# Optimization experiments

Measured on AMD Instinct MI355X. Metric: run time of the kernel, lower is better.

Reference implementation:

```python
import jax, jax.numpy as jnp
import numpy as np

V, E, H = 50257, 256, 128          # vocab, embedding_size, lstm hidden per direction
L, B = 2048, 64                    # seq_len, batch (x is [L, B], seq-first)
SEP, MASK = 50256, 0
SEP_EVERY = 16
N_UTT = L // SEP_EVERY             # utterances per sequence (seps planted regularly)


def setup_inputs() -> dict:
    key = jax.random.key(0)
    ks = jax.random.split(key, 12)
    x = jax.random.randint(ks[0], (L, B), 0, SEP, dtype=jnp.int32)
    # plant sep tokens every SEP_EVERY positions -> each utterance has SEP_EVERY tokens
    x = x.at[SEP_EVERY - 1::SEP_EVERY, :].set(SEP)
    s = 1.0 / np.sqrt(H)
    u = lambda k, sh: jax.random.uniform(k, sh, jnp.float32, -s, s)
    return {
        "x": x,
        "emb": jax.random.normal(ks[1], (V, E), jnp.float32),
        "w_ih_f": u(ks[2], (4 * H, E)), "w_hh_f": u(ks[3], (4 * H, H)),
        "b_ih_f": u(ks[4], (4 * H,)),   "b_hh_f": u(ks[5], (4 * H,)),
        "w_ih_b": u(ks[6], (4 * H, E)), "w_hh_b": u(ks[7], (4 * H, H)),
        "b_ih_b": u(ks[8], (4 * H,)),   "b_hh_b": u(ks[9], (4 * H,)),
        "w_out": u(ks[10], (2, E)),     "b_out": u(ks[11], (2,)),
    }


def _lstm_dir(xu, w_ih, w_hh, b_ih, b_hh, reverse):
    # xu: [T, B, E]; PyTorch LSTM gate order i, f, g, o
    xp = jnp.einsum("tbe,ge->tbg", xu, w_ih) + b_ih + b_hh  # [T, B, 4H]

    def step(carry, xt):
        h, c = carry
        g = xt + h @ w_hh.T
        i, f, gg, o = jnp.split(g, 4, axis=-1)
        c = jax.nn.sigmoid(f) * c + jax.nn.sigmoid(i) * jnp.tanh(gg)
        h = jax.nn.sigmoid(o) * jnp.tanh(c)
        return (h, c), h

    init = (jnp.zeros((xu.shape[1], H), xu.dtype), jnp.zeros((xu.shape[1], H), xu.dtype))
    _, hs = jax.lax.scan(step, init, xp, reverse=reverse)
    return hs  # [T, B, H]


def _forward(x, emb, w_ih_f, w_hh_f, b_ih_f, b_hh_f, w_ih_b, w_hh_b, b_ih_b, b_hh_b, w_out, b_out):
    # --- ragged utterance mean-pool (replaces per-token Python loops) ---
    seps = (x == SEP)
    seg = jnp.cumsum(seps.astype(jnp.int32), axis=0) - seps.astype(jnp.int32)  # [L,B]: utterance id per token (sep ends its utterance)
    gids = (seg * B + jnp.arange(B, dtype=jnp.int32)[None, :]).reshape(L * B)
    tok_emb = emb[x]                                              # [L, B, E]
    sums = jax.ops.segment_sum(tok_emb.reshape(L * B, E), gids, num_segments=N_UTT * B).reshape(N_UTT, B, E)
    cnts = jax.ops.segment_sum(jnp.ones((L * B,), tok_emb.dtype), gids, num_segments=N_UTT * B).reshape(N_UTT, B, 1)
    u = jnp.where(cnts > 0, sums / jnp.maximum(cnts, 1.0), 0.0)   # [N_UTT, B, E] (zeros pad, as original)
    # --- BiLSTM over utterances ---
    h_f = _lstm_dir(u, w_ih_f, w_hh_f, b_ih_f, b_hh_f, reverse=False)
    h_b = _lstm_dir(u, w_ih_b, w_hh_b, b_ih_b, b_hh_b, reverse=True)
    h = jnp.concatenate([h_f, h_b], axis=-1)                      # [N_UTT, B, E]
    logits = jnp.einsum("tbe,oe->tbo", h, w_out) + b_out          # [N_UTT, B, 2]
    policy = jax.nn.softmax(logits, axis=-1)
    # greedy policy (deterministic reference)
    u_mask = jnp.argmax(policy, axis=-1)                          # [N_UTT, B] in {0,1}
    chosen_policy = jnp.take_along_axis(policy, u_mask[..., None], axis=-1)  # [N_UTT, B, 1]
    # expand utterance mask to token mask and mask the input
    token_mask = u_mask.astype(bool)[seg, jnp.arange(B)[None, :]]  # [L, B]
    masked_input = jnp.where(token_mask, x, MASK)
    return logits, policy, chosen_policy, u_mask.astype(bool), masked_input


def reference(x, emb, w_ih_f, w_hh_f, b_ih_f, b_hh_f, w_ih_b, w_hh_b, b_ih_b, b_hh_b, w_out, b_out):
    return _forward(x, emb, w_ih_f, w_hh_f, b_ih_f, b_hh_f, w_ih_b, w_hh_b, b_ih_b, b_hh_b, w_out, b_out)
```

## Files before the change

### kernel.cpp

```cpp
#include <hip/hip_runtime.h>
#include <hip/hip_fp16.h>
#include <math.h>

#define LL   2048
#define BB   64
#define EE   256
#define HH   128
#define GG   512
#define TT   128
#define SEPT 50256

__global__ __launch_bounds__(256) void segscan_k(
    const int* __restrict__ x, int* __restrict__ seg,
    int* __restrict__ cnt, int* __restrict__ start)
{
    int b   = blockIdx.x;
    int tid = threadIdx.x;
    __shared__ int tsum[256];
    __shared__ int ucnt[TT];
    __shared__ int ustart[TT];

    int flags[8];
    int local = 0;
#pragma unroll
    for (int i = 0; i < 8; i++) {
        int t = tid * 8 + i;
        flags[i] = (x[t * BB + b] == SEPT) ? 1 : 0;
        local += flags[i];
    }
    tsum[tid] = local;
    __syncthreads();
    int val = local;
    for (int off = 1; off < 256; off <<= 1) {
        int other = (tid >= off) ? tsum[tid - off] : 0;
        __syncthreads();
        val += other;
        tsum[tid] = val;
        __syncthreads();
    }
    int excl = val - local;

    if (tid < TT) ucnt[tid] = 0;
    __syncthreads();
    int run = excl;
#pragma unroll
    for (int i = 0; i < 8; i++) {
        int t = tid * 8 + i;
        int s = run;
        seg[t * BB + b] = s;
        run += flags[i];
        if (s < TT) atomicAdd(&ucnt[s], 1);
    }
    __syncthreads();
    if (tid == 0) {
        int acc = 0;
        for (int u = 0; u < TT; u++) { ustart[u] = acc; acc += ucnt[u]; }
    }
    __syncthreads();
    if (tid < TT) {
        cnt[tid * BB + b]   = ucnt[tid];
        start[tid * BB + b] = ustart[tid];
    }
}

__global__ __launch_bounds__(256) void pool_k(
    const int* __restrict__ x, const float* __restrict__ emb,
    const int* __restrict__ cnt, const int* __restrict__ start,
    float* __restrict__ up)
{
    int wid  = threadIdx.x >> 6;
    int lane = threadIdx.x & 63;
    int bid  = blockIdx.x * 4 + wid;
    int b    = bid & 63;
    int c    = cnt[bid];
    int st   = start[bid];

    float4 acc = {0.f, 0.f, 0.f, 0.f};
    int tok = (c > 0) ? x[st * BB + b] : 0;
    for (int j = 0; j < c; j++) {
        int tok_n = (j + 1 < c) ? x[(st + j + 1) * BB + b] : 0;
        float4 v = ((const float4*)(emb + (size_t)tok * EE))[lane];
        acc.x += v.x; acc.y += v.y; acc.z += v.z; acc.w += v.w;
        tok = tok_n;
    }
    float inv = (c > 0) ? 1.f / (float)c : 0.f;
    float4 r = {acc.x * inv, acc.y * inv, acc.z * inv, acc.w * inv};
    ((float4*)(up + (size_t)bid * EE))[lane] = r;
}

__global__ __launch_bounds__(256) void xp_gemm_k(
    const float* __restrict__ A,
    const float* __restrict__ wf, const float* __restrict__ wb,
    const float* __restrict__ bihf, const float* __restrict__ bhhf,
    const float* __restrict__ bihb, const float* __restrict__ bhhb,
    float* __restrict__ C)
{
    __shared__ float As[32][128];
    __shared__ float Bs[32][128];
    int tid  = threadIdx.x;
    int row0 = blockIdx.x * 128;
    int col0 = blockIdx.y * 128;
    int tx = tid & 15, ty = tid >> 4;
    float acc[8][8] = {};

    for (int k0 = 0; k0 < EE; k0 += 32) {
#pragma unroll
        for (int i = 0; i < 4; i++) {
            int idx = tid + i * 256;
            int m   = idx >> 3;
            int k4  = idx & 7;
            float4 av = *(const float4*)(A + (size_t)(row0 + m) * EE + k0 + k4 * 4);
            As[k4 * 4 + 0][m] = av.x; As[k4 * 4 + 1][m] = av.y;
            As[k4 * 4 + 2][m] = av.z; As[k4 * 4 + 3][m] = av.w;
        }
#pragma unroll
        for (int i = 0; i < 4; i++) {
            int idx = tid + i * 256;
            int n   = idx >> 3;
            int k4  = idx & 7;
            int gc  = col0 + n;
            const float* wsrc = (gc < GG) ? (wf + (size_t)gc * EE)
                                          : (wb + (size_t)(gc - GG) * EE);
            float4 bv = *(const float4*)(wsrc + k0 + k4 * 4);
            Bs[k4 * 4 + 0][n] = bv.x; Bs[k4 * 4 + 1][n] = bv.y;
            Bs[k4 * 4 + 2][n] = bv.z; Bs[k4 * 4 + 3][n] = bv.w;
        }
        __syncthreads();
#pragma unroll
        for (int k = 0; k < 32; k++) {
            float a8[8], b8[8];
            *(float4*)&a8[0] = *(const float4*)&As[k][ty * 8 + 0];
            *(float4*)&a8[4] = *(const float4*)&As[k][ty * 8 + 4];
            *(float4*)&b8[0] = *(const float4*)&Bs[k][tx * 8 + 0];
            *(float4*)&b8[4] = *(const float4*)&Bs[k][tx * 8 + 4];
#pragma unroll
            for (int i = 0; i < 8; i++)
#pragma unroll
                for (int j = 0; j < 8; j++)
                    acc[i][j] += a8[i] * b8[j];
        }
        __syncthreads();
    }

    float bias[8];
#pragma unroll
    for (int j = 0; j < 8; j++) {
        int gc = col0 + tx * 8 + j;
        bias[j] = (gc < GG) ? (bihf[gc] + bhhf[gc])
                            : (bihb[gc - GG] + bhhb[gc - GG]);
    }
#pragma unroll
    for (int i = 0; i < 8; i++) {
        int r = row0 + ty * 8 + i;
        float4 v0 = {acc[i][0] + bias[0], acc[i][1] + bias[1],
                     acc[i][2] + bias[2], acc[i][3] + bias[3]};
        float4 v1 = {acc[i][4] + bias[4], acc[i][5] + bias[5],
                     acc[i][6] + bias[6], acc[i][7] + bias[7]};
        *(float4*)(C + (size_t)r * 1024 + col0 + tx * 8 + 0) = v0;
        *(float4*)(C + (size_t)r * 1024 + col0 + tx * 8 + 4) = v1;
    }
}

__device__ __forceinline__ float sigm_f(float x) {
    return 1.f / (1.f + __expf(-x));
}
__device__ __forceinline__ float tanh_f(float x) {
    return 1.f - 2.f / (__expf(2.f * x) + 1.f);
}

__global__ __launch_bounds__(256) void cvt_k(
    const float* __restrict__ wf, const float* __restrict__ wb,
    __half* __restrict__ o)
{
    int i = blockIdx.x * 256 + threadIdx.x;
    int e   = i & 7;
    int g   = (i >> 3) & 511;
    int q   = (i >> 12) & 15;
    int dir = i >> 16;
    const float* src = dir ? wb : wf;
    o[i] = __float2half(src[(size_t)g * HH + q * 8 + e]);
}

typedef _Float16 h2v __attribute__((ext_vector_type(2)));
__device__ __forceinline__ float dot2h(unsigned wbits, unsigned hbits, float c) {
    return __builtin_amdgcn_fdot2(__builtin_bit_cast(h2v, wbits),
                                  __builtin_bit_cast(h2v, hbits), c, false);
}

__global__ __launch_bounds__(512, 2) void lstm_rec_k(
    const float* __restrict__ xp,
    const __half* __restrict__ w16,
    float* __restrict__ hout)
{
    int bid = blockIdx.x;
    int dir = bid >> 6;
    int b   = bid & 63;
    int tid = threadIdx.x;
    int g   = tid;
    int sect = g >> 7;
    const uint4* wp = (const uint4*)(w16 + (size_t)dir * (16 * GG * 8));

    __shared__ uint4 wlds[8 * GG];
    __shared__ __align__(16) __half h16_lds[HH];
    __shared__ float act[GG];

#pragma unroll
    for (int t = 0; t < 8; t++) {
        int idx = tid + t * 512;
        wlds[idx] = wp[idx];
    }

    float c = 0.f;
    if (tid < HH) h16_lds[tid] = __float2half(0.f);
    __syncthreads();

    const uint4* h16v = (const uint4*)h16_lds;

    int t0   = dir ? (TT - 1) : 0;
    float xg = xp[(size_t)(t0 * BB + b) * 1024 + dir * GG + g];

    for (int s = 0; s < TT; s++) {
        uint4 q8[8];
#pragma unroll
        for (int q = 0; q < 8; q++)
            q8[q] = wp[(q + 8) * GG + g];

        float acc = xg;
#pragma unroll
        for (int q = 0; q < 8; q++) {
            uint4 w = wlds[q * GG + g];
            uint4 hv = h16v[q];
            acc = dot2h(w.x, hv.x, acc);
            acc = dot2h(w.y, hv.y, acc);
            acc = dot2h(w.z, hv.z, acc);
            acc = dot2h(w.w, hv.w, acc);
        }
#pragma unroll
        for (int q = 0; q < 8; q++) {
            uint4 w = q8[q];
            uint4 hv = h16v[q + 8];
            acc = dot2h(w.x, hv.x, acc);
            acc = dot2h(w.y, hv.y, acc);
            acc = dot2h(w.z, hv.z, acc);
            acc = dot2h(w.w, hv.w, acc);
        }

        act[g] = (sect == 2) ? tanh_f(acc) : sigm_f(acc);

        float xg_next = xg;
        if (s < TT - 1) {
            int tn = dir ? (TT - 2 - s) : (s + 1);
            xg_next = xp[(size_t)(tn * BB + b) * 1024 + dir * GG + g];
        }
        __syncthreads();

        if (tid < HH) {
            float si = act[tid], sf = act[HH + tid];
            float tg = act[2 * HH + tid], so = act[3 * HH + tid];
            c = sf * c + si * tg;
            float h = so * tanh_f(c);
            h16_lds[tid] = __float2half(h);
            int t = dir ? (TT - 1 - s) : s;
            hout[((size_t)(dir * TT + t) * BB + b) * HH + tid] = h;
        }
        xg = xg_next;
        __syncthreads();
    }
}

__global__ __launch_bounds__(256) void head_k(
    const float* __restrict__ hbuf,
    const float* __restrict__ wout, const float* __restrict__ bout,
    float* __restrict__ out)
{
    int wid  = threadIdx.x >> 6;
    int lane = threadIdx.x & 63;
    int row  = blockIdx.x * 4 + wid;
    int t = row >> 6, b = row & 63;
    const float* hf = hbuf + ((size_t)(t)      * BB + b) * HH;
    const float* hb = hbuf + ((size_t)(TT + t) * BB + b) * HH;

    float l0 = 0.f, l1 = 0.f, v;
    v = hf[lane];      l0 += v * wout[lane];           l1 += v * wout[256 + lane];
    v = hf[lane + 64]; l0 += v * wout[64 + lane];      l1 += v * wout[320 + lane];
    v = hb[lane];      l0 += v * wout[128 + lane];     l1 += v * wout[384 + lane];
    v = hb[lane + 64]; l0 += v * wout[192 + lane];     l1 += v * wout[448 + lane];
#pragma unroll
    for (int off = 32; off > 0; off >>= 1) {
        l0 += __shfl_down(l0, off);
        l1 += __shfl_down(l1, off);
    }
    if (lane == 0) {
        l0 += bout[0]; l1 += bout[1];
        float m  = fmaxf(l0, l1);
        float e0 = __expf(l0 - m), e1 = __expf(l1 - m);
        float inv = 1.f / (e0 + e1);
        float p0 = e0 * inv, p1 = e1 * inv;
        int amax = (l1 > l0) ? 1 : 0;
        out[(size_t)row * 2 + 0] = l0;
        out[(size_t)row * 2 + 1] = l1;
        out[16384 + (size_t)row * 2 + 0] = p0;
        out[16384 + (size_t)row * 2 + 1] = p1;
        out[32768 + row] = amax ? p1 : p0;
        out[40960 + row] = (float)amax;
    }
}

__global__ __launch_bounds__(256) void mask_k(
    const int* __restrict__ x, const int* __restrict__ seg,
    const float* __restrict__ umask, float* __restrict__ out4)
{
    int idx = blockIdx.x * 256 + threadIdx.x;
    int b = idx & 63;
    int s = seg[idx];
    if (s > TT - 1) s = TT - 1;
    if (s < 0) s = 0;
    float keep = umask[s * BB + b];
    out4[idx] = (keep != 0.f) ? (float)x[idx] : 0.f;
}

extern "C" void kernel_launch(void* const* d_in, const int* in_sizes, int n_in,
                              void* d_out, int out_size, void* d_ws, size_t ws_size,
                              hipStream_t stream)
{
    const int*   x    = (const int*)  d_in[0];
    const float* emb  = (const float*)d_in[1];
    const float* wihf = (const float*)d_in[2];
    const float* whhf = (const float*)d_in[3];
    const float* bihf = (const float*)d_in[4];
    const float* bhhf = (const float*)d_in[5];
    const float* wihb = (const float*)d_in[6];
    const float* whhb = (const float*)d_in[7];
    const float* bihb = (const float*)d_in[8];
    const float* bhhb = (const float*)d_in[9];
    const float* wout = (const float*)d_in[10];
    const float* bout = (const float*)d_in[11];
    float* out = (float*)d_out;
    char*  ws  = (char*)d_ws;

    int*   seg   = (int*)  (ws + 0);
    int*   cnt   = (int*)  (ws + 524288);
    int*   start = (int*)  (ws + 557056);
    float* up    = (float*)(ws + 589824);
    float* xp    = (float*)(ws + 8978432);
    float* hbuf  = (float*)(ws + 42532864);
    __half* wh16 = (__half*)up;

    segscan_k<<<64, 256, 0, stream>>>(x, seg, cnt, start);
    pool_k<<<2048, 256, 0, stream>>>(x, emb, cnt, start, up);
    xp_gemm_k<<<dim3(64, 8), 256, 0, stream>>>(up, wihf, wihb, bihf, bhhf, bihb, bhhb, xp);
    cvt_k<<<512, 256, 0, stream>>>(whhf, whhb, wh16);
    lstm_rec_k<<<128, 512, 0, stream>>>(xp, wh16, hbuf);
    head_k<<<2048, 256, 0, stream>>>(hbuf, wout, bout, out);
    mask_k<<<512, 256, 0, stream>>>(x, seg, out + 40960, out + 49152);
}
```

Baseline: 288.1 us.

## Interleave LSTM gates per hidden unit and use shuffles with double-buffered h

```diff
diff --git a/kernel.cpp b/kernel.cpp
--- a/kernel.cpp
+++ b/kernel.cpp
@@ -174,9 +174,12 @@
 {
     int i = blockIdx.x * 256 + threadIdx.x;
     int e   = i & 7;
-    int g   = (i >> 3) & 511;
+    int p   = (i >> 3) & 511;
     int q   = (i >> 12) & 15;
     int dir = i >> 16;
+    int j   = p & 3;
+    int u   = p >> 2;
+    int g   = j * HH + u;
     const float* src = dir ? wb : wf;
     o[i] = __float2half(src[(size_t)g * HH + q * 8 + e]);
 }
@@ -196,13 +199,13 @@
     int dir = bid >> 6;
     int b   = bid & 63;
     int tid = threadIdx.x;
-    int g   = tid;
-    int sect = g >> 7;
+    int j   = tid & 3;
+    int u   = tid >> 2;
+    int g   = j * HH + u;
     const uint4* wp = (const uint4*)(w16 + (size_t)dir * (16 * GG * 8));
 
     __shared__ uint4 wlds[8 * GG];
-    __shared__ __align__(16) __half h16_lds[HH];
-    __shared__ float act[GG];
+    __shared__ __align__(16) __half hb2[2][HH];
 
 #pragma unroll
     for (int t = 0; t < 8; t++) {
@@ -211,59 +214,58 @@
     }
 
     float c = 0.f;
-    if (tid < HH) h16_lds[tid] = __float2half(0.f);
-    __syncthreads();
-
-    const uint4* h16v = (const uint4*)h16_lds;
-
-    int t0   = dir ? (TT - 1) : 0;
+    if (tid < HH) hb2[0][tid] = __float2half(0.f);
+    __syncthreads();
+
+    int t0 = dir ? (TT - 1) : 0;
     float xg = xp[(size_t)(t0 * BB + b) * 1024 + dir * GG + g];
 
+    int pb = 0;
     for (int s = 0; s < TT; s++) {
-        uint4 q8[8];
-#pragma unroll
-        for (int q = 0; q < 8; q++)
-            q8[q] = wp[(q + 8) * GG + g];
+        const uint4* hv = (const uint4*)hb2[pb];
 
         float acc = xg;
 #pragma unroll
         for (int q = 0; q < 8; q++) {
-            uint4 w = wlds[q * GG + g];
-            uint4 hv = h16v[q];
-            acc = dot2h(w.x, hv.x, acc);
-            acc = dot2h(w.y, hv.y, acc);
-            acc = dot2h(w.z, hv.z, acc);
-            acc = dot2h(w.w, hv.w, acc);
+            uint4 w  = wlds[q * 512 + tid];
+            uint4 h4 = hv[q];
+            acc = dot2h(w.x, h4.x, acc);
+            acc = dot2h(w.y, h4.y, acc);
+            acc = dot2h(w.z, h4.z, acc);
+            acc = dot2h(w.w, h4.w, acc);
         }
 #pragma unroll
         for (int q = 0; q < 8; q++) {
-            uint4 w = q8[q];
-            uint4 hv = h16v[q + 8];
-            acc = dot2h(w.x, hv.x, acc);
-            acc = dot2h(w.y, hv.y, acc);
-            acc = dot2h(w.z, hv.z, acc);
-            acc = dot2h(w.w, hv.w, acc);
-        }
-
-        act[g] = (sect == 2) ? tanh_f(acc) : sigm_f(acc);
+            uint4 w  = wp[(q + 8) * 512 + tid];
+            uint4 h4 = hv[q + 8];
+            acc = dot2h(w.x, h4.x, acc);
+            acc = dot2h(w.y, h4.y, acc);
+            acc = dot2h(w.z, h4.z, acc);
+            acc = dot2h(w.w, h4.w, acc);
+        }
+
+        float ex = __expf((j == 2) ? 2.f * acc : -acc);
+        float a  = (j == 2) ? (1.f - 2.f / (ex + 1.f)) : (1.f / (1.f + ex));
+
+        float a1 = __shfl_down(a, 1);
+        float a2 = __shfl_down(a, 2);
+        float a3 = __shfl_down(a, 3);
 
         float xg_next = xg;
         if (s < TT - 1) {
             int tn = dir ? (TT - 2 - s) : (s + 1);
             xg_next = xp[(size_t)(tn * BB + b) * 1024 + dir * GG + g];
         }
-        __syncthreads();
-
-        if (tid < HH) {
-            float si = act[tid], sf = act[HH + tid];
-            float tg = act[2 * HH + tid], so = act[3 * HH + tid];
-            c = sf * c + si * tg;
-            float h = so * tanh_f(c);
-            h16_lds[tid] = __float2half(h);
+
+        if (j == 0) {
+            c = a1 * c + a * a2;
+            float h = a3 * tanh_f(c);
+            hb2[pb ^ 1][u] = __float2half(h);
             int t = dir ? (TT - 1 - s) : s;
-            hout[((size_t)(dir * TT + t) * BB + b) * HH + tid] = h;
+            hout[((size_t)(dir * TT + t) * BB + b) * HH + u] = h;
         }
         xg = xg_next;
+        pb ^= 1;
         __syncthreads();
     }
 }
```

Measured after the change: 296.1 us. 1.03x slower.
